# Kernel tuning notes

Measured on AMD Instinct MI355X. Metric: run time of the kernel, lower is better.

## Reference

```python
import jax, jax.numpy as jnp
from jax import lax
import numpy as np

N_CLUSTERS = 8
G_CLUSTERS = 2
D_DIM = 512
DN = ('NCHW', 'OIHW', 'NCHW')


def _conv(x, w, b):
    y = lax.conv_general_dilated(x, w, window_strides=(1, 1), padding='VALID',
                                 dimension_numbers=DN)
    return y + b[None, :, None, None]


def setup_inputs() -> dict:
    key = jax.random.key(0)
    ks = jax.random.split(key, 6)
    B, D, H, W = 32, D_DIM, 7, 250
    KG = N_CLUSTERS + G_CLUSTERS
    scale = 1.0 / np.sqrt(D * 7)
    return {
        'x': jax.random.normal(ks[0], (B, D, H, W), dtype=jnp.float32),
        'feat_w': jax.random.normal(ks[1], (D, D, 7, 1), dtype=jnp.float32) * scale,
        'feat_b': jax.random.normal(ks[2], (D,), dtype=jnp.float32) * 0.01,
        'assign_w': jax.random.normal(ks[3], (KG, D, 7, 1), dtype=jnp.float32) * scale,
        'assign_b': jax.random.normal(ks[4], (KG,), dtype=jnp.float32) * 0.01,
        'centroids': jax.random.uniform(ks[5], (D, KG), dtype=jnp.float32),
    }


def reference(x, feat_w, feat_b, assign_w, assign_b, centroids):
    # features branch: conv(7,1) + ReLU -> (B, D, H', W)
    feat = jnp.maximum(_conv(x, feat_w, feat_b), 0.0)
    # assignment branch: conv(7,1) -> softmax over clusters -> (B, K+G, H', W)
    soft = jax.nn.softmax(_conv(x, assign_w, assign_b), axis=1)
    # Fused VLAD aggregation (mathematically identical to
    # sum_hw soft[b,k,hw] * (feat[b,d,hw] - centroids[d,k]) without
    # materializing the (B,D,K+G,H',W) residual tensor):
    s_sum = soft.sum(axis=(-2, -1))                                # (B, K+G)
    agg = jnp.einsum('bkhw,bdhw->bdk', soft, feat)                 # (B, D, K+G)
    cluster_res = agg - centroids[None, :, :] * s_sum[:, None, :]  # (B, D, K+G)
    cluster_res = cluster_res[..., :N_CLUSTERS]                    # drop ghost clusters
    # L2 normalize over feature dim (torch F.normalize, eps=1e-12)
    norm = jnp.sqrt(jnp.sum(cluster_res * cluster_res, axis=1, keepdims=True))
    cluster_l2 = cluster_res / jnp.maximum(norm, 1e-12)
    # (B, D, K) -> (B, K, D) -> (B, K*D)
    out = jnp.swapaxes(cluster_l2, 1, 2).reshape(x.shape[0], N_CLUSTERS * D_DIM)
    return out
```

## Files before the change

### kernel.cpp

```cpp
#include <hip/hip_runtime.h>
#include <stdint.h>

typedef float f32x4 __attribute__((ext_vector_type(4)));
typedef __bf16 bf16x8 __attribute__((ext_vector_type(8)));
typedef unsigned short ushortx8 __attribute__((ext_vector_type(8)));

#define D_DIM 512
#define KGC 10
#define NCLU 8
#define BATCH 32
#define WPOS 250
#define WPAD 256
#define KDIM 3584
#define MROWS 522
#define MPAD 528
#define MBIG 640
#define BM 160
#define BN 128
#define KSPLIT 2
#define KCHUNK 1792
#define NS 28
#define NT 64

#define ASM_VMCNT16() asm volatile("s_waitcnt vmcnt(16)" ::: "memory")
#define ASM_VMCNT0()  asm volatile("s_waitcnt vmcnt(0)" ::: "memory")
#define ASM_LGKM0()   asm volatile("s_waitcnt lgkmcnt(0)" ::: "memory")
#define BAR() do { __builtin_amdgcn_s_barrier(); __builtin_amdgcn_sched_barrier(0); } while (0)

__device__ __forceinline__ float bf2f(unsigned short u) {
  union { unsigned int i; float f; } v; v.i = ((unsigned int)u) << 16; return v.f;
}
__device__ __forceinline__ unsigned short f2bf(float f) {
  union { float f; unsigned int i; } v; v.f = f;
  unsigned int r = v.i + 0x7FFFu + ((v.i >> 16) & 1u);
  return (unsigned short)(r >> 16);
}

__device__ __forceinline__ void load_lds16(const void* g, void* l) {
  __builtin_amdgcn_global_load_lds(
      (const __attribute__((address_space(1))) void*)g,
      (__attribute__((address_space(3))) void*)l, 16, 0, 0);
}

__global__ void prep_kernel(const float* __restrict__ fw,
                            const float* __restrict__ fb,
                            const float* __restrict__ aw,
                            const float* __restrict__ ab,
                            unsigned short* __restrict__ Wcat,
                            float* __restrict__ bcat) {
  int r = blockIdx.x;
  unsigned short* dst = Wcat + (size_t)r * KDIM;
  const float* src = (r < D_DIM) ? (fw + (size_t)r * KDIM)
                   : (r < MROWS) ? (aw + (size_t)(r - D_DIM) * KDIM)
                                 : nullptr;
  for (int i = threadIdx.x; i < KDIM / 4; i += 256) {
    unsigned short o0 = 0, o1 = 0, o2 = 0, o3 = 0;
    if (src) {
      float4 v = ((const float4*)src)[i];
      o0 = f2bf(v.x); o1 = f2bf(v.y); o2 = f2bf(v.z); o3 = f2bf(v.w);
    }
    ushort4 o; o.x = o0; o.y = o1; o.z = o2; o.w = o3;
    ((ushort4*)dst)[i] = o;
  }
  if (threadIdx.x == 0)
    bcat[r] = r < D_DIM ? fb[r] : (r < MROWS ? ab[r - D_DIM] : 0.f);
}

__global__ __launch_bounds__(512, 4) void gemm_fused(
    const float* __restrict__ x, const unsigned short* __restrict__ Wcat,
    float* __restrict__ P) {
  __shared__ __align__(16) unsigned short Wl[2][BM * 64];
  __shared__ __align__(16) unsigned short Xl[2][BN * 64];
  const int tid = threadIdx.x;
  const int nt = blockIdx.x, mh = blockIdx.y, sp = blockIdx.z;
  const int lane = tid & 63, wv = tid >> 6;
  const int wm = wv >> 2, wn = wv & 3;
  const int fr = lane & 15, kg = lane >> 4;
  const int sx = fr & 7;
  const int nloc = tid & 127, oc = tid >> 7;
  const int nglob = nt * BN + nloc;
  const int b = nglob >> 8, ncol = nglob & 255;
  const bool okn = ncol < WPOS;
  const float* xb = x + (size_t)b * KDIM * WPOS + ncol;
  const int kbase = sp * KCHUNK;
  const unsigned short* Wg = Wcat + (size_t)mh * BM * KDIM + kbase;

  float xr[16];
  auto loadx = [&](int st) {
#pragma unroll
    for (int pass = 0; pass < 2; pass++) {
      int k0 = kbase + st * 64 + (oc + 4 * pass) * 8;
#pragma unroll
      for (int e = 0; e < 8; e++)
        xr[pass * 8 + e] = okn ? xb[(size_t)(k0 + e) * WPOS] : 0.f;
    }
  };
  auto stageW = [&](int st, int buf) {
#pragma unroll
    for (int it = 0; it < 3; it++) {
      int s = (it < 2) ? it * 512 + tid : 1024 + (tid & 255);
      int row = s >> 3, p = s & 7;
      int blk = p ^ (row & 7);
      load_lds16(Wg + (size_t)row * KDIM + st * 64 + blk * 8, &Wl[buf][s * 8]);
    }
  };
  auto writeX = [&](int buf) {
#pragma unroll
    for (int pass = 0; pass < 2; pass++) {
      int oct = oc + 4 * pass;
      ushortx8 pk;
#pragma unroll
      for (int e = 0; e < 8; e++) pk[e] = f2bf(xr[pass * 8 + e]);
      *(ushortx8*)&Xl[buf][nloc * 64 + (oct ^ (nloc & 7)) * 8] = pk;
    }
  };

  f32x4 acc[5][2];
  const f32x4 zero = {0.f, 0.f, 0.f, 0.f};
#pragma unroll
  for (int f = 0; f < 5; f++) { acc[f][0] = zero; acc[f][1] = zero; }

  loadx(0);
  stageW(0, 0);
  writeX(0);
  loadx(1);
  ASM_VMCNT16();
  ASM_LGKM0();
  BAR();

  for (int t = 0; t < NS; ++t) {
    const int cur = t & 1, nxt = cur ^ 1;
    const bool more = (t + 1 < NS);
    if (more) {
      stageW(t + 1, nxt);
      writeX(nxt);
    }
    if (t + 2 < NS) loadx(t + 2);
#pragma unroll
    for (int ks = 0; ks < 2; ks++) {
      const int off = ((ks * 4 + kg) ^ sx) * 8;
      bf16x8 b0 = *(const bf16x8*)&Xl[cur][(wn * 32 + fr) * 64 + off];
      bf16x8 b1 = *(const bf16x8*)&Xl[cur][(wn * 32 + 16 + fr) * 64 + off];
#pragma unroll
      for (int f = 0; f < 5; f++) {
        bf16x8 af = *(const bf16x8*)&Wl[cur][(wm * 80 + f * 16 + fr) * 64 + off];
        acc[f][0] = __builtin_amdgcn_mfma_f32_16x16x32_bf16(af, b0, acc[f][0], 0, 0, 0);
        acc[f][1] = __builtin_amdgcn_mfma_f32_16x16x32_bf16(af, b1, acc[f][1], 0, 0, 0);
      }
    }
    if (more) {
      if (t + 2 < NS) { ASM_VMCNT16(); }
      else            { ASM_VMCNT0();  }
      ASM_LGKM0();
      BAR();
    }
  }

  float* Pb = P + (size_t)((sp * 4 + mh) * NT + nt) * (BM * BN);
#pragma unroll
  for (int f = 0; f < 5; f++) {
    const int m = wm * 80 + f * 16 + kg * 4;
#pragma unroll
    for (int nf = 0; nf < 2; nf++) {
      const int n = wn * 32 + nf * 16 + fr;
#pragma unroll
      for (int r = 0; r < 4; r++)
        Pb[(size_t)(m + r) * BN + n] = acc[f][nf][r];
    }
  }
}

__global__ __launch_bounds__(256) void reduce_kernel(
    const float* __restrict__ P, const float* __restrict__ bcat,
    unsigned short* __restrict__ Y) {
  const int nt = blockIdx.x, mg = blockIdx.y;
  const int t = threadIdx.x;
  const int m = mg * 16 + (t >> 4);
  const int nl = (t & 15) * 8;
  if (m >= MPAD) return;
  const int mh = (m >= 480) ? 3 : (m >= 320) ? 2 : (m >= 160) ? 1 : 0;
  const int ml = m - mh * BM;
  const size_t slice = (size_t)BM * BN;
  const size_t base = (size_t)ml * BN + nl;
  float s[8];
#pragma unroll
  for (int e = 0; e < 8; e++) s[e] = 0.f;
#pragma unroll
  for (int sp = 0; sp < KSPLIT; sp++) {
    const float* p = P + ((size_t)((sp * 4 + mh) * NT) + nt) * slice + base;
    float4 a = *(const float4*)p;
    float4 c = *(const float4*)(p + 4);
    s[0] += a.x; s[1] += a.y; s[2] += a.z; s[3] += a.w;
    s[4] += c.x; s[5] += c.y; s[6] += c.z; s[7] += c.w;
  }
  float bias = bcat[m];
  ushortx8 o;
#pragma unroll
  for (int e = 0; e < 8; e++) {
    float v = s[e] + bias;
    if (m < D_DIM) v = fmaxf(v, 0.f);
    o[e] = f2bf(v);
  }
  const int nglob = nt * BN + nl;
  const int bb = nglob >> 8, col = nglob & 255;
  *(ushortx8*)&Y[(size_t)bb * MPAD * WPAD + (size_t)m * WPAD + col] = o;
}

__global__ __launch_bounds__(512) void epi_kernel(
    const unsigned short* __restrict__ Y, const float* __restrict__ cent,
    float* __restrict__ out) {
  __shared__ float soft[WPAD];
  __shared__ float red[8];
  const int b = blockIdx.x >> 3, k = blockIdx.x & 7;
  const int tid = threadIdx.x;
  const unsigned short* Yb = Y + (size_t)b * MPAD * WPAD;

  float sv = 0.f;
  if (tid < WPOS) {
    float lg[KGC];
    float mx = -1e30f;
#pragma unroll
    for (int j = 0; j < KGC; j++) {
      lg[j] = bf2f(Yb[(size_t)(D_DIM + j) * WPAD + tid]);
      mx = fmaxf(mx, lg[j]);
    }
    float s = 0.f, ek = 0.f;
#pragma unroll
    for (int j = 0; j < KGC; j++) {
      float e = __expf(lg[j] - mx);
      s += e;
      if (j == k) ek = e;
    }
    sv = ek / s;
  }
  if (tid < WPAD) soft[tid] = sv;
  __syncthreads();

  float v = sv;
#pragma unroll
  for (int o = 32; o > 0; o >>= 1) v += __shfl_down(v, o, 64);
  if ((tid & 63) == 0) red[tid >> 6] = v;
  __syncthreads();
  float ssum = 0.f;
#pragma unroll
  for (int i = 0; i < 8; i++) ssum += red[i];

  float a[8];
#pragma unroll
  for (int u = 0; u < 8; u++) a[u] = 0.f;
  const unsigned short* row = Yb + (size_t)tid * WPAD;
  for (int w = 0; w < WPAD; w += 8) {
    ushortx8 f0 = *(const ushortx8*)(row + w);
    float4 s0 = *(const float4*)&soft[w];
    float4 s1 = *(const float4*)&soft[w + 4];
    a[0] += bf2f(f0[0]) * s0.x;
    a[1] += bf2f(f0[1]) * s0.y;
    a[2] += bf2f(f0[2]) * s0.z;
    a[3] += bf2f(f0[3]) * s0.w;
    a[4] += bf2f(f0[4]) * s1.x;
    a[5] += bf2f(f0[5]) * s1.y;
    a[6] += bf2f(f0[6]) * s1.z;
    a[7] += bf2f(f0[7]) * s1.w;
  }
  float asum = ((a[0] + a[1]) + (a[2] + a[3])) + ((a[4] + a[5]) + (a[6] + a[7]));
  float c = asum - cent[(size_t)tid * KGC + k] * ssum;

  __syncthreads();
  float q = c * c;
#pragma unroll
  for (int o = 32; o > 0; o >>= 1) q += __shfl_down(q, o, 64);
  if ((tid & 63) == 0) red[tid >> 6] = q;
  __syncthreads();
  float nsum = 0.f;
#pragma unroll
  for (int i = 0; i < 8; i++) nsum += red[i];
  float norm = sqrtf(nsum);
  float inv = 1.f / fmaxf(norm, 1e-12f);

  float* ob = out + (size_t)b * (NCLU * D_DIM) + (size_t)k * D_DIM;
  ob[tid] = c * inv;
}

extern "C" void kernel_launch(void* const* d_in, const int* in_sizes, int n_in,
                              void* d_out, int out_size, void* d_ws, size_t ws_size,
                              hipStream_t stream) {
  const float* x  = (const float*)d_in[0];
  const float* fw = (const float*)d_in[1];
  const float* fb = (const float*)d_in[2];
  const float* aw = (const float*)d_in[3];
  const float* ab = (const float*)d_in[4];
  const float* ce = (const float*)d_in[5];
  float* out = (float*)d_out;
  char* ws = (char*)d_ws;

  const size_t WC_BYTES = (size_t)MBIG * KDIM * 2;
  const size_t BC_BYTES = 4096;
  const size_t P_BYTES  = (size_t)KSPLIT * 4 * NT * BM * BN * 4;
  unsigned short* Wc = (unsigned short*)(ws);
  float*          bc = (float*)(ws + WC_BYTES);
  float*          P  = (float*)(ws + WC_BYTES + BC_BYTES);
  unsigned short* Yv = (unsigned short*)(ws + WC_BYTES + BC_BYTES + P_BYTES);

  prep_kernel<<<MBIG, 256, 0, stream>>>(fw, fb, aw, ab, Wc, bc);
  gemm_fused<<<dim3(NT, 4, KSPLIT), 512, 0, stream>>>(x, Wc, P);
  reduce_kernel<<<dim3(NT, 40), 256, 0, stream>>>(P, bc, Yv);
  epi_kernel<<<BATCH * NCLU, 512, 0, stream>>>(Yv, ce, out);
}
```

Baseline: 251.5 us.

## Pre-pack x into MFMA fragment layout in prep kernel, load B directly to registers

Result: no change. 250.8 us (-0.3%).

```diff
diff --git a/kernel.cpp b/kernel.cpp
--- a/kernel.cpp
+++ b/kernel.cpp
@@ -21,11 +21,8 @@
 #define KCHUNK 1792
 #define NS 28
 #define NT 64
-
-#define ASM_VMCNT16() asm volatile("s_waitcnt vmcnt(16)" ::: "memory")
-#define ASM_VMCNT0()  asm volatile("s_waitcnt vmcnt(0)" ::: "memory")
-#define ASM_LGKM0()   asm volatile("s_waitcnt lgkmcnt(0)" ::: "memory")
-#define BAR() do { __builtin_amdgcn_s_barrier(); __builtin_amdgcn_sched_barrier(0); } while (0)
+#define KSG 56
+#define XTILE 8192
 
 __device__ __forceinline__ float bf2f(unsigned short u) {
   union { unsigned int i; float f; } v; v.i = ((unsigned int)u) << 16; return v.f;
@@ -42,77 +39,89 @@
       (__attribute__((address_space(3))) void*)l, 16, 0, 0);
 }
 
-__global__ void prep_kernel(const float* __restrict__ fw,
-                            const float* __restrict__ fb,
-                            const float* __restrict__ aw,
-                            const float* __restrict__ ab,
-                            unsigned short* __restrict__ Wcat,
-                            float* __restrict__ bcat) {
-  int r = blockIdx.x;
-  unsigned short* dst = Wcat + (size_t)r * KDIM;
-  const float* src = (r < D_DIM) ? (fw + (size_t)r * KDIM)
-                   : (r < MROWS) ? (aw + (size_t)(r - D_DIM) * KDIM)
-                                 : nullptr;
-  for (int i = threadIdx.x; i < KDIM / 4; i += 256) {
-    unsigned short o0 = 0, o1 = 0, o2 = 0, o3 = 0;
-    if (src) {
-      float4 v = ((const float4*)src)[i];
-      o0 = f2bf(v.x); o1 = f2bf(v.y); o2 = f2bf(v.z); o3 = f2bf(v.w);
-    }
-    ushort4 o; o.x = o0; o.y = o1; o.z = o2; o.w = o3;
-    ((ushort4*)dst)[i] = o;
-  }
-  if (threadIdx.x == 0)
-    bcat[r] = r < D_DIM ? fb[r] : (r < MROWS ? ab[r - D_DIM] : 0.f);
+__global__ __launch_bounds__(256) void prep2_kernel(
+    const float* __restrict__ fw, const float* __restrict__ fb,
+    const float* __restrict__ aw, const float* __restrict__ ab,
+    const float* __restrict__ x,
+    unsigned short* __restrict__ Wcat, float* __restrict__ bcat,
+    unsigned short* __restrict__ XS) {
+  const int bid = blockIdx.x;
+  const int tid = threadIdx.x;
+  if (bid < MBIG) {
+    int r = bid;
+    unsigned short* dst = Wcat + (size_t)r * KDIM;
+    const float* src = (r < D_DIM) ? (fw + (size_t)r * KDIM)
+                     : (r < MROWS) ? (aw + (size_t)(r - D_DIM) * KDIM)
+                                   : nullptr;
+    for (int i = tid; i < KDIM / 4; i += 256) {
+      unsigned short o0 = 0, o1 = 0, o2 = 0, o3 = 0;
+      if (src) {
+        float4 v = ((const float4*)src)[i];
+        o0 = f2bf(v.x); o1 = f2bf(v.y); o2 = f2bf(v.z); o3 = f2bf(v.w);
+      }
+      ushort4 o; o.x = o0; o.y = o1; o.z = o2; o.w = o3;
+      ((ushort4*)dst)[i] = o;
+    }
+    if (tid == 0)
+      bcat[r] = r < D_DIM ? fb[r] : (r < MROWS ? ab[r - D_DIM] : 0.f);
+  } else {
+    const int xt = bid - MBIG;
+    const int nt = xt / KSG, ksg = xt - nt * KSG;
+    unsigned short* tb = XS + (size_t)(nt * KSG + ksg) * XTILE;
+#pragma unroll
+    for (int i = 0; i < 4; i++) {
+      const int L = tid + 256 * i;
+      const int ks = L >> 9, nf = (L >> 6) & 7, lane = L & 63;
+      const int fr = lane & 15, kg = lane >> 4;
+      const int n = nt * 128 + nf * 16 + fr;
+      const int b = n >> 8, col = n & 255;
+      const int k0 = ksg * 64 + ks * 32 + kg * 8;
+      const float* xp = x + ((size_t)b * KDIM + k0) * WPOS + col;
+      ushortx8 pk;
+      if (col < WPOS) {
+#pragma unroll
+        for (int e = 0; e < 8; e++) pk[e] = f2bf(xp[(size_t)e * WPOS]);
+      } else {
+#pragma unroll
+        for (int e = 0; e < 8; e++) pk[e] = 0;
+      }
+      *(ushortx8*)&tb[(size_t)L * 8] = pk;
+    }
+  }
 }
 
 __global__ __launch_bounds__(512, 4) void gemm_fused(
-    const float* __restrict__ x, const unsigned short* __restrict__ Wcat,
+    const unsigned short* __restrict__ XS, const unsigned short* __restrict__ Wcat,
     float* __restrict__ P) {
   __shared__ __align__(16) unsigned short Wl[2][BM * 64];
-  __shared__ __align__(16) unsigned short Xl[2][BN * 64];
   const int tid = threadIdx.x;
   const int nt = blockIdx.x, mh = blockIdx.y, sp = blockIdx.z;
   const int lane = tid & 63, wv = tid >> 6;
   const int wm = wv >> 2, wn = wv & 3;
   const int fr = lane & 15, kg = lane >> 4;
   const int sx = fr & 7;
-  const int nloc = tid & 127, oc = tid >> 7;
-  const int nglob = nt * BN + nloc;
-  const int b = nglob >> 8, ncol = nglob & 255;
-  const bool okn = ncol < WPOS;
-  const float* xb = x + (size_t)b * KDIM * WPOS + ncol;
-  const int kbase = sp * KCHUNK;
-  const unsigned short* Wg = Wcat + (size_t)mh * BM * KDIM + kbase;
-
-  float xr[16];
-  auto loadx = [&](int st) {
-#pragma unroll
-    for (int pass = 0; pass < 2; pass++) {
-      int k0 = kbase + st * 64 + (oc + 4 * pass) * 8;
-#pragma unroll
-      for (int e = 0; e < 8; e++)
-        xr[pass * 8 + e] = okn ? xb[(size_t)(k0 + e) * WPOS] : 0.f;
+  const unsigned short* Wg = Wcat + (size_t)mh * BM * KDIM + sp * KCHUNK;
+  const unsigned short* xsb = XS + (size_t)nt * (KSG * XTILE)
+                                 + (size_t)sp * NS * XTILE
+                                 + (wn * 1024 + lane * 8);
+
+  auto stageW = [&](int st, int buf) {
+#pragma unroll
+    for (int it = 0; it < 3; it++) {
+      int s = it * 512 + tid;
+      if (s < BM * 8) {
+        int row = s >> 3, p = s & 7;
+        int blk = p ^ (row & 7);
+        load_lds16(Wg + (size_t)row * KDIM + st * 64 + blk * 8, &Wl[buf][s * 8]);
+      }
     }
   };
-  auto stageW = [&](int st, int buf) {
-#pragma unroll
-    for (int it = 0; it < 3; it++) {
-      int s = (it < 2) ? it * 512 + tid : 1024 + (tid & 255);
-      int row = s >> 3, p = s & 7;
-      int blk = p ^ (row & 7);
-      load_lds16(Wg + (size_t)row * KDIM + st * 64 + blk * 8, &Wl[buf][s * 8]);
-    }
-  };
-  auto writeX = [&](int buf) {
-#pragma unroll
-    for (int pass = 0; pass < 2; pass++) {
-      int oct = oc + 4 * pass;
-      ushortx8 pk;
-#pragma unroll
-      for (int e = 0; e < 8; e++) pk[e] = f2bf(xr[pass * 8 + e]);
-      *(ushortx8*)&Xl[buf][nloc * 64 + (oct ^ (nloc & 7)) * 8] = pk;
-    }
+  auto loadX = [&](int st, bf16x8& x0, bf16x8& x1, bf16x8& x2, bf16x8& x3) {
+    const unsigned short* p = xsb + (size_t)st * XTILE;
+    x0 = *(const bf16x8*)(p);
+    x1 = *(const bf16x8*)(p + 512);
+    x2 = *(const bf16x8*)(p + 4096);
+    x3 = *(const bf16x8*)(p + 4096 + 512);
   };
 
   f32x4 acc[5][2];
@@ -120,40 +129,39 @@
 #pragma unroll
   for (int f = 0; f < 5; f++) { acc[f][0] = zero; acc[f][1] = zero; }
 
-  loadx(0);
-  stageW(0, 0);
-  writeX(0);
-  loadx(1);
-  ASM_VMCNT16();
-  ASM_LGKM0();
-  BAR();
-
-  for (int t = 0; t < NS; ++t) {
-    const int cur = t & 1, nxt = cur ^ 1;
-    const bool more = (t + 1 < NS);
-    if (more) {
-      stageW(t + 1, nxt);
-      writeX(nxt);
-    }
-    if (t + 2 < NS) loadx(t + 2);
+  auto compute = [&](const unsigned short* wb, bf16x8 xa, bf16x8 xb,
+                     bf16x8 xc, bf16x8 xd) {
 #pragma unroll
     for (int ks = 0; ks < 2; ks++) {
+      bf16x8 b0 = ks ? xc : xa;
+      bf16x8 b1 = ks ? xd : xb;
       const int off = ((ks * 4 + kg) ^ sx) * 8;
-      bf16x8 b0 = *(const bf16x8*)&Xl[cur][(wn * 32 + fr) * 64 + off];
-      bf16x8 b1 = *(const bf16x8*)&Xl[cur][(wn * 32 + 16 + fr) * 64 + off];
 #pragma unroll
       for (int f = 0; f < 5; f++) {
-        bf16x8 af = *(const bf16x8*)&Wl[cur][(wm * 80 + f * 16 + fr) * 64 + off];
+        bf16x8 af = *(const bf16x8*)&wb[(wm * 80 + f * 16 + fr) * 64 + off];
         acc[f][0] = __builtin_amdgcn_mfma_f32_16x16x32_bf16(af, b0, acc[f][0], 0, 0, 0);
         acc[f][1] = __builtin_amdgcn_mfma_f32_16x16x32_bf16(af, b1, acc[f][1], 0, 0, 0);
       }
     }
-    if (more) {
-      if (t + 2 < NS) { ASM_VMCNT16(); }
-      else            { ASM_VMCNT0();  }
-      ASM_LGKM0();
-      BAR();
-    }
+  };
+
+  bf16x8 xA0, xA1, xA2, xA3, xB0, xB1, xB2, xB3;
+
+  stageW(0, 0);
+  loadX(0, xA0, xA1, xA2, xA3);
+  __syncthreads();
+
+  for (int t = 0; t < NS; t += 2) {
+    stageW(t + 1, 1);
+    loadX(t + 1, xB0, xB1, xB2, xB3);
+    compute(Wl[0], xA0, xA1, xA2, xA3);
+    __syncthreads();
+    if (t + 2 < NS) {
+      stageW(t + 2, 0);
+      loadX(t + 2, xA0, xA1, xA2, xA3);
+    }
+    compute(Wl[1], xB0, xB1, xB2, xB3);
+    __syncthreads();
   }
 
   float* Pb = P + (size_t)((sp * 4 + mh) * NT + nt) * (BM * BN);
@@ -296,13 +304,15 @@
   const size_t WC_BYTES = (size_t)MBIG * KDIM * 2;
   const size_t BC_BYTES = 4096;
   const size_t P_BYTES  = (size_t)KSPLIT * 4 * NT * BM * BN * 4;
+  const size_t XS_BYTES = (size_t)NT * KSG * XTILE * 2;
   unsigned short* Wc = (unsigned short*)(ws);
   float*          bc = (float*)(ws + WC_BYTES);
   float*          P  = (float*)(ws + WC_BYTES + BC_BYTES);
-  unsigned short* Yv = (unsigned short*)(ws + WC_BYTES + BC_BYTES + P_BYTES);
-
-  prep_kernel<<<MBIG, 256, 0, stream>>>(fw, fb, aw, ab, Wc, bc);
-  gemm_fused<<<dim3(NT, 4, KSPLIT), 512, 0, stream>>>(x, Wc, P);
+  unsigned short* XSp= (unsigned short*)(ws + WC_BYTES + BC_BYTES + P_BYTES);
+  unsigned short* Yv = XSp;
+
+  prep2_kernel<<<MBIG + NT * KSG, 256, 0, stream>>>(fw, fb, aw, ab, x, Wc, bc, XSp);
+  gemm_fused<<<dim3(NT, 4, KSPLIT), 512, 0, stream>>>(XSp, Wc, P);
   reduce_kernel<<<dim3(NT, 40), 256, 0, stream>>>(P, bc, Yv);
   epi_kernel<<<BATCH * NCLU, 512, 0, stream>>>(Yv, ce, out);
 }
```
